# Kernel optimization log

Measured on AMD Instinct MI355X. Metric: run time of the kernel, lower is better.

The kernel has to match this reference:

```python
import jax, jax.numpy as jnp
import numpy as np

B, T, C, H = 2, 2048, 1024, 16
HD = C // H
EPS = 1e-5


def _gelu_tanh(x):
    # 0.5*x*(1+tanh(sqrt(2/pi)*(x+0.044715*x^3)))
    c = jnp.sqrt(jnp.asarray(2.0 / np.pi, dtype=x.dtype))
    return 0.5 * x * (1.0 + jnp.tanh(c * (x + 0.044715 * x * x * x)))


def _layernorm(x, g, b):
    mu = jnp.mean(x, axis=-1, keepdims=True)
    var = jnp.mean(jnp.square(x - mu), axis=-1, keepdims=True)
    return (x - mu) * jax.lax.rsqrt(var + EPS) * g + b


def setup_inputs() -> dict:
    key = jax.random.key(0)
    ks = jax.random.split(key, 8)
    s = lambda fan_in: 1.0 / np.sqrt(fan_in)
    return {
        "x": jax.random.normal(ks[0], (B, T, C), jnp.float32),
        "ln1_g": jnp.ones((C,), jnp.float32),
        "ln1_b": jnp.zeros((C,), jnp.float32),
        "W_attn": jax.random.normal(ks[1], (C, 3 * C), jnp.float32) * s(C),
        "b_attn": jnp.zeros((3 * C,), jnp.float32),
        "W_proj": jax.random.normal(ks[2], (C, C), jnp.float32) * s(C),
        "b_proj": jnp.zeros((C,), jnp.float32),
        "ln2_g": jnp.ones((C,), jnp.float32),
        "ln2_b": jnp.zeros((C,), jnp.float32),
        "W_fc": jax.random.normal(ks[3], (C, 4 * C), jnp.float32) * s(C),
        "b_fc": jnp.zeros((4 * C,), jnp.float32),
        "W_fc2": jax.random.normal(ks[4], (4 * C, C), jnp.float32) * s(4 * C),
        "b_fc2": jnp.zeros((C,), jnp.float32),
    }


def reference(x, ln1_g, ln1_b, W_attn, b_attn, W_proj, b_proj,
              ln2_g, ln2_b, W_fc, b_fc, W_fc2, b_fc2):
    # --- attention branch (pre-LN) ---
    h = _layernorm(x, ln1_g, ln1_b)
    qkv = h @ W_attn + b_attn                      # [B,T,3C]
    q, k, v = jnp.split(qkv, 3, axis=2)
    q = q.reshape(B, T, H, HD).transpose(0, 2, 1, 3)  # [B,H,T,HD]
    k = k.reshape(B, T, H, HD).transpose(0, 2, 1, 3)
    v = v.reshape(B, T, H, HD).transpose(0, 2, 1, 3)
    att = jnp.einsum('bhqd,bhkd->bhqk', q, k) / jnp.sqrt(jnp.asarray(HD, x.dtype))
    causal = jnp.tril(jnp.ones((T, T), bool))
    att = jnp.where(causal, att, jnp.asarray(-jnp.inf, att.dtype))
    att = jax.nn.softmax(att, axis=-1)
    y = jnp.einsum('bhqk,bhkd->bhqd', att, v)      # [B,H,T,HD]
    y = y.transpose(0, 2, 1, 3).reshape(B, T, C)
    x = x + (y @ W_proj + b_proj)
    # --- MLP branch (pre-LN) ---
    h = _layernorm(x, ln2_g, ln2_b)
    h = _gelu_tanh(h @ W_fc + b_fc)
    x = x + (h @ W_fc2 + b_fc2)
    return x
```

## Files before the change

kernel.cpp:

```cpp
#include <hip/hip_runtime.h>
#include <hip/hip_bf16.h>
#include <cstdint>
#include <cstddef>

#define B_  2
#define T_  2048
#define C_  1024
#define H_  16
#define HD_ 64
#define M_TOT 4096

typedef __bf16 bf16x8 __attribute__((ext_vector_type(8)));
typedef float  f32x4  __attribute__((ext_vector_type(4)));
typedef unsigned short u16;

__device__ __forceinline__ u16 f2bf(float f) {
  __hip_bfloat16 h = __float2bfloat16(f);
  return __builtin_bit_cast(u16, h);
}

__device__ __forceinline__ void async_cp16(const u16* g, u16* l) {
  __builtin_amdgcn_global_load_lds(
      (const __attribute__((address_space(1))) void*)g,
      (__attribute__((address_space(3))) void*)l, 16, 0, 0);
}

__device__ __forceinline__ float gelu_f(float x) {
  const float z = 0.7978845608028654f * (x + 0.044715f * x * x * x);
  return x / (1.0f + __expf(-2.0f * z));
}

__global__ __launch_bounds__(256) void ln_bf16_kernel(
    const float* __restrict__ x, const float* __restrict__ g,
    const float* __restrict__ b, u16* __restrict__ out) {
  const int row = blockIdx.x;
  const int tid = threadIdx.x;
  const float4 v = reinterpret_cast<const float4*>(x)[row * 256 + tid];
  float s  = v.x + v.y + v.z + v.w;
  float sq = v.x * v.x + v.y * v.y + v.z * v.z + v.w * v.w;
#pragma unroll
  for (int off = 32; off > 0; off >>= 1) {
    s  += __shfl_xor(s, off);
    sq += __shfl_xor(sq, off);
  }
  __shared__ float red[8];
  const int wave = tid >> 6;
  if ((tid & 63) == 0) { red[wave] = s; red[4 + wave] = sq; }
  __syncthreads();
  s  = red[0] + red[1] + red[2] + red[3];
  sq = red[4] + red[5] + red[6] + red[7];
  const float mu   = s * (1.0f / 1024.0f);
  const float rstd = rsqrtf(sq * (1.0f / 1024.0f) - mu * mu + 1e-5f);
  const float4 gv = reinterpret_cast<const float4*>(g)[tid];
  const float4 bv = reinterpret_cast<const float4*>(b)[tid];
  ushort4 o;
  o.x = f2bf((v.x - mu) * rstd * gv.x + bv.x);
  o.y = f2bf((v.y - mu) * rstd * gv.y + bv.y);
  o.z = f2bf((v.z - mu) * rstd * gv.z + bv.z);
  o.w = f2bf((v.w - mu) * rstd * gv.w + bv.w);
  reinterpret_cast<ushort4*>(out)[row * 256 + tid] = o;
}

__global__ __launch_bounds__(256) void transpose_bf16_kernel(
    const float* __restrict__ W, u16* __restrict__ Wt, int K, int N) {
  __shared__ float tile[32][33];
  const int n0 = blockIdx.x * 32, k0 = blockIdx.y * 32;
  const int tx = threadIdx.x & 31;
  const int ty = threadIdx.x >> 5;
#pragma unroll
  for (int i = 0; i < 4; ++i)
    tile[ty + 8 * i][tx] = W[(k0 + ty + 8 * i) * (size_t)N + n0 + tx];
  __syncthreads();
#pragma unroll
  for (int i = 0; i < 4; ++i)
    Wt[(n0 + ty + 8 * i) * (size_t)K + k0 + tx] = f2bf(tile[tx][ty + 8 * i]);
}

template <int MODE, int BM>
__global__ __launch_bounds__(256, 2) void gemm_kernel(
    const u16* __restrict__ A, const u16* __restrict__ Bt,
    const float* __restrict__ bias, const float* __restrict__ resid,
    float* __restrict__ outf, u16* __restrict__ outb,
    u16* __restrict__ qo, u16* __restrict__ ko, u16* __restrict__ vto,
    int M, int N, int K, int logPer) {
  constexpr int MT = BM / 32;
  constexpr int AI = BM / 32;
  __shared__ __align__(16) u16 As[BM * 64];
  __shared__ __align__(16) u16 Bs[128 * 64];
  const int tid  = threadIdx.x;
  const int wave = tid >> 6, lane = tid & 63;
  const int col  = lane & 15, quad = lane >> 4;
  const int wm   = wave >> 1, wn = wave & 1;

  const int flat = blockIdx.y * gridDim.x + blockIdx.x;
  const int xcd = flat & 7, sl = flat >> 3;
  const int per = 1 << logPer;
  const int bm = (xcd << logPer) + (sl & (per - 1));
  const int bn = sl >> logPer;

  const int srow = lane >> 3, sc8 = lane & 7;
  const int kcs = (sc8 ^ srow) * 8;
  const u16* ap = A  + (size_t)(bm * BM + wave * (BM / 4) + srow) * K + kcs;
  const u16* bp = Bt + (size_t)(bn * 128 + wave * 32 + srow) * K + kcs;
  u16* as_dst = As + wave * (BM / 4) * 64;
  u16* bs_dst = Bs + wave * 2048;

  f32x4 acc[MT][4] = {};

  for (int k0 = 0; k0 < K; k0 += 64) {
    __syncthreads();
#pragma unroll
    for (int i = 0; i < AI; ++i)
      async_cp16(ap + k0 + i * 8 * (size_t)K, as_dst + i * 512);
#pragma unroll
    for (int i = 0; i < 4; ++i)
      async_cp16(bp + k0 + i * 8 * (size_t)K, bs_dst + i * 512);
    __syncthreads();
#pragma unroll
    for (int kh = 0; kh < 2; ++kh) {
      const int ks = kh * 4;
      bf16x8 af[MT], bf[4];
#pragma unroll
      for (int mt = 0; mt < MT; ++mt) {
        const int row = wm * (BM / 2) + mt * 16 + col;
        af[mt] = *reinterpret_cast<const bf16x8*>(&As[row * 64 + ((ks + quad) ^ (col & 7)) * 8]);
      }
#pragma unroll
      for (int nt = 0; nt < 4; ++nt) {
        const int row = wn * 64 + nt * 16 + col;
        bf[nt] = *reinterpret_cast<const bf16x8*>(&Bs[row * 64 + ((ks + quad) ^ (col & 7)) * 8]);
      }
#pragma unroll
      for (int mt = 0; mt < MT; ++mt)
#pragma unroll
        for (int nt = 0; nt < 4; ++nt)
          acc[mt][nt] = __builtin_amdgcn_mfma_f32_16x16x32_bf16(af[mt], bf[nt], acc[mt][nt], 0, 0, 0);
    }
  }

#pragma unroll
  for (int mt = 0; mt < MT; ++mt) {
#pragma unroll
    for (int r = 0; r < 4; ++r) {
      const int grow = bm * BM + wm * (BM / 2) + mt * 16 + quad * 4 + r;
#pragma unroll
      for (int nt = 0; nt < 4; ++nt) {
        const int gcol = bn * 128 + wn * 64 + nt * 16 + col;
        const float val = acc[mt][nt][r] + bias[gcol];
        if constexpr (MODE == 0) {
          outb[(size_t)grow * N + gcol] = f2bf(gelu_f(val));
        } else if constexpr (MODE == 1) {
          outf[(size_t)grow * N + gcol] = resid[(size_t)grow * N + gcol] + val;
        } else {
          const int which = gcol >> 10, c = gcol & 1023;
          const int hh = c >> 6, dd = c & 63;
          const int bb = grow >> 11, tt = grow & 2047;
          if (which == 0)
            qo[((bb * H_ + hh) * (size_t)T_ + tt) * HD_ + dd] = f2bf(val * 0.125f);
          else if (which == 1)
            ko[((bb * H_ + hh) * (size_t)T_ + tt) * HD_ + dd] = f2bf(val);
          else
            vto[((bb * H_ + hh) * (size_t)HD_ + dd) * T_ + tt] = f2bf(val);
        }
      }
    }
  }
}

#define PSTR 68
__global__ __launch_bounds__(256, 4) void attn_kernel(
    const u16* __restrict__ q, const u16* __restrict__ k,
    const u16* __restrict__ vt, u16* __restrict__ y) {
  const int bh  = blockIdx.x;
  const int qt  = (T_ / 64 - 1) - blockIdx.y;
  const int tid = threadIdx.x;
  const int wave = tid >> 6, lane = tid & 63;
  const int col = lane & 15, quad = lane >> 4;
  const int b = bh >> 4, h = bh & 15;
  const int r0w = qt * 64 + wave * 16;

  __shared__ __align__(16) u16 Klds[64 * PSTR];
  __shared__ __align__(16) u16 Vtlds[64 * PSTR];
  __shared__ __align__(16) u16 Plds[4 * 16 * PSTR];

  bf16x8 aq[2];
#pragma unroll
  for (int j = 0; j < 2; ++j)
    aq[j] = *reinterpret_cast<const bf16x8*>(
        &q[((size_t)bh * T_ + r0w + col) * HD_ + j * 32 + quad * 8]);

  bf16x8 ones;
#pragma unroll
  for (int jj = 0; jj < 8; ++jj) ones[jj] = (__bf16)1.0f;

  f32x4 o[4] = {};
  f32x4 l_acc = {};

  const int srow = tid >> 3, spart = tid & 7;
  u16* pw = Plds + wave * 16 * PSTR;
  const u16* kbase  = k  + (size_t)bh * T_ * HD_ + srow * HD_ + spart * 8;
  const u16* vtbase = vt + (size_t)bh * HD_ * T_ + srow * T_ + spart * 8;

  const int kb_last = qt * 64;

  uint4 kv0, kv1, kv2, kv3;
  kv0 = *reinterpret_cast<const uint4*>(kbase);
  kv1 = *reinterpret_cast<const uint4*>(kbase + 32 * HD_);
  kv2 = *reinterpret_cast<const uint4*>(vtbase);
  kv3 = *reinterpret_cast<const uint4*>(vtbase + 32 * T_);

  for (int kb = 0; kb <= kb_last; kb += 64) {
    *reinterpret_cast<uint4*>(&Klds[srow * PSTR + spart * 8])        = kv0;
    *reinterpret_cast<uint4*>(&Klds[(srow + 32) * PSTR + spart * 8]) = kv1;
    *reinterpret_cast<uint4*>(&Vtlds[srow * PSTR + spart * 8])        = kv2;
    *reinterpret_cast<uint4*>(&Vtlds[(srow + 32) * PSTR + spart * 8]) = kv3;
    __syncthreads();

    if (kb < kb_last) {
      const int nk = kb + 64;
      kv0 = *reinterpret_cast<const uint4*>(kbase + (size_t)nk * HD_);
      kv1 = *reinterpret_cast<const uint4*>(kbase + (size_t)nk * HD_ + 32 * HD_);
      kv2 = *reinterpret_cast<const uint4*>(vtbase + nk);
      kv3 = *reinterpret_cast<const uint4*>(vtbase + 32 * T_ + nk);
    }

    f32x4 s[4];
#pragma unroll
    for (int n = 0; n < 4; ++n) {
      const bf16x8 bk0 = *reinterpret_cast<const bf16x8*>(&Klds[(n * 16 + col) * PSTR + quad * 8]);
      const bf16x8 bk1 = *reinterpret_cast<const bf16x8*>(&Klds[(n * 16 + col) * PSTR + 32 + quad * 8]);
      f32x4 z = {};
      z = __builtin_amdgcn_mfma_f32_16x16x32_bf16(aq[0], bk0, z, 0, 0, 0);
      s[n] = __builtin_amdgcn_mfma_f32_16x16x32_bf16(aq[1], bk1, z, 0, 0, 0);
    }

    const bool domask = (kb == kb_last);
#pragma unroll
    for (int n = 0; n < 4; ++n) {
#pragma unroll
      for (int r = 0; r < 4; ++r) {
        float sv = s[n][r];
        if (domask) {
          const int key = kb + n * 16 + col;
          const int row = r0w + quad * 4 + r;
          sv = (key <= row) ? sv : -1e30f;
        }
        pw[(quad * 4 + r) * PSTR + n * 16 + col] = f2bf(__expf(sv));
      }
    }
    __builtin_amdgcn_s_waitcnt(0xC07F);

    const bf16x8 ap0 = *reinterpret_cast<const bf16x8*>(&pw[col * PSTR + quad * 8]);
    const bf16x8 ap1 = *reinterpret_cast<const bf16x8*>(&pw[col * PSTR + 32 + quad * 8]);
    l_acc = __builtin_amdgcn_mfma_f32_16x16x32_bf16(ap0, ones, l_acc, 0, 0, 0);
    l_acc = __builtin_amdgcn_mfma_f32_16x16x32_bf16(ap1, ones, l_acc, 0, 0, 0);
#pragma unroll
    for (int n = 0; n < 4; ++n) {
      const bf16x8 bv0 = *reinterpret_cast<const bf16x8*>(&Vtlds[(n * 16 + col) * PSTR + quad * 8]);
      const bf16x8 bv1 = *reinterpret_cast<const bf16x8*>(&Vtlds[(n * 16 + col) * PSTR + 32 + quad * 8]);
      o[n] = __builtin_amdgcn_mfma_f32_16x16x32_bf16(ap0, bv0, o[n], 0, 0, 0);
      o[n] = __builtin_amdgcn_mfma_f32_16x16x32_bf16(ap1, bv1, o[n], 0, 0, 0);
    }
    __syncthreads();
  }

#pragma unroll
  for (int r = 0; r < 4; ++r) {
    const int qrow = r0w + quad * 4 + r;
    const float inv = 1.0f / l_acc[r];
#pragma unroll
    for (int n = 0; n < 4; ++n)
      y[((size_t)b * T_ + qrow) * C_ + h * HD_ + n * 16 + col] = f2bf(o[n][r] * inv);
  }
}

extern "C" void kernel_launch(void* const* d_in, const int* in_sizes, int n_in,
                              void* d_out, int out_size, void* d_ws, size_t ws_size,
                              hipStream_t stream) {
  const float* x      = (const float*)d_in[0];
  const float* ln1_g  = (const float*)d_in[1];
  const float* ln1_b  = (const float*)d_in[2];
  const float* W_attn = (const float*)d_in[3];
  const float* b_attn = (const float*)d_in[4];
  const float* W_proj = (const float*)d_in[5];
  const float* b_proj = (const float*)d_in[6];
  const float* ln2_g  = (const float*)d_in[7];
  const float* ln2_b  = (const float*)d_in[8];
  const float* W_fc   = (const float*)d_in[9];
  const float* b_fc   = (const float*)d_in[10];
  const float* W_fc2  = (const float*)d_in[11];
  const float* b_fc2  = (const float*)d_in[12];
  float* out = (float*)d_out;

  char* p = (char*)d_ws;
  auto alloc = [&](size_t bytes) {
    char* r = p;
    p += (bytes + 255) & ~(size_t)255;
    return r;
  };
  u16*   h1      = (u16*)alloc((size_t)M_TOT * C_ * 2);
  u16*   wt_attn = (u16*)alloc((size_t)3 * C_ * C_ * 2);
  u16*   wt_proj = (u16*)alloc((size_t)C_ * C_ * 2);
  u16*   wt_fc   = (u16*)alloc((size_t)4 * C_ * C_ * 2);
  u16*   wt_fc2  = (u16*)alloc((size_t)C_ * 4 * C_ * 2);
  u16*   qbuf    = (u16*)alloc((size_t)M_TOT * C_ * 2);
  u16*   kbuf    = (u16*)alloc((size_t)M_TOT * C_ * 2);
  u16*   vtbuf   = (u16*)alloc((size_t)M_TOT * C_ * 2);
  u16*   ybuf    = (u16*)alloc((size_t)M_TOT * C_ * 2);
  float* x2      = (float*)alloc((size_t)M_TOT * C_ * 4);
  u16*   h2      = (u16*)alloc((size_t)M_TOT * C_ * 2);
  u16*   act     = (u16*)alloc((size_t)M_TOT * 4 * C_ * 2);

  transpose_bf16_kernel<<<dim3(96, 32),  256, 0, stream>>>(W_attn, wt_attn, 1024, 3072);
  transpose_bf16_kernel<<<dim3(32, 32),  256, 0, stream>>>(W_proj, wt_proj, 1024, 1024);
  transpose_bf16_kernel<<<dim3(128, 32), 256, 0, stream>>>(W_fc,   wt_fc,   1024, 4096);
  transpose_bf16_kernel<<<dim3(32, 128), 256, 0, stream>>>(W_fc2,  wt_fc2,  4096, 1024);

  ln_bf16_kernel<<<M_TOT, 256, 0, stream>>>(x, ln1_g, ln1_b, h1);

  gemm_kernel<3, 128><<<dim3(24, 32), 256, 0, stream>>>(h1, wt_attn, b_attn, nullptr,
                                                        nullptr, nullptr, qbuf, kbuf, vtbuf,
                                                        4096, 3072, 1024, 2);
  attn_kernel<<<dim3(32, 32), 256, 0, stream>>>(qbuf, kbuf, vtbuf, ybuf);

  gemm_kernel<1, 64><<<dim3(8, 64), 256, 0, stream>>>(ybuf, wt_proj, b_proj, x,
                                                      x2, nullptr, nullptr, nullptr, nullptr,
                                                      4096, 1024, 1024, 3);
  ln_bf16_kernel<<<M_TOT, 256, 0, stream>>>(x2, ln2_g, ln2_b, h2);

  gemm_kernel<0, 128><<<dim3(32, 32), 256, 0, stream>>>(h2, wt_fc, b_fc, nullptr,
                                                        nullptr, act, nullptr, nullptr, nullptr,
                                                        4096, 4096, 1024, 2);
  gemm_kernel<1, 64><<<dim3(8, 64), 256, 0, stream>>>(act, wt_fc2, b_fc2, x2,
                                                      out, nullptr, nullptr, nullptr, nullptr,
                                                      4096, 1024, 4096, 3);
}
```

Before: 338.4 us.

## Load K and V tiles directly from global memory, drop shared staging

The attention kernel no longer stages K and V^T tiles through shared memory with block-wide barriers and register prefetch. Each wave now loads its MFMA operands for K and V^T straight from global memory, relying on L1/L2 to serve the four waves that read the same tile. This removes both __syncthreads per iteration and the LDS write/read traffic, and lowers occupancy hints from 4 to 3 blocks per SU. The cost is fourfold redundant global/cache traffic per block and no software prefetch, so load latency is exposed unless other waves hide it.

```diff
diff --git a/kernel.cpp b/kernel.cpp
--- a/kernel.cpp
+++ b/kernel.cpp
@@ -168,7 +168,7 @@
 }
 
 #define PSTR 68
-__global__ __launch_bounds__(256, 4) void attn_kernel(
+__global__ __launch_bounds__(256, 3) void attn_kernel(
     const u16* __restrict__ q, const u16* __restrict__ k,
     const u16* __restrict__ vt, u16* __restrict__ y) {
   const int bh  = blockIdx.x;
@@ -179,9 +179,8 @@
   const int b = bh >> 4, h = bh & 15;
   const int r0w = qt * 64 + wave * 16;
 
-  __shared__ __align__(16) u16 Klds[64 * PSTR];
-  __shared__ __align__(16) u16 Vtlds[64 * PSTR];
   __shared__ __align__(16) u16 Plds[4 * 16 * PSTR];
+  u16* pw = Plds + wave * 16 * PSTR;
 
   bf16x8 aq[2];
 #pragma unroll
@@ -196,42 +195,33 @@
   f32x4 o[4] = {};
   f32x4 l_acc = {};
 
-  const int srow = tid >> 3, spart = tid & 7;
-  u16* pw = Plds + wave * 16 * PSTR;
-  const u16* kbase  = k  + (size_t)bh * T_ * HD_ + srow * HD_ + spart * 8;
-  const u16* vtbase = vt + (size_t)bh * HD_ * T_ + srow * T_ + spart * 8;
+  const u16* kb_ptr = k  + ((size_t)bh * T_ + col) * HD_ + quad * 8;
+  const u16* vb_ptr = vt + ((size_t)bh * HD_ + col) * T_ + quad * 8;
 
   const int kb_last = qt * 64;
 
-  uint4 kv0, kv1, kv2, kv3;
-  kv0 = *reinterpret_cast<const uint4*>(kbase);
-  kv1 = *reinterpret_cast<const uint4*>(kbase + 32 * HD_);
-  kv2 = *reinterpret_cast<const uint4*>(vtbase);
-  kv3 = *reinterpret_cast<const uint4*>(vtbase + 32 * T_);
-
   for (int kb = 0; kb <= kb_last; kb += 64) {
-    *reinterpret_cast<uint4*>(&Klds[srow * PSTR + spart * 8])        = kv0;
-    *reinterpret_cast<uint4*>(&Klds[(srow + 32) * PSTR + spart * 8]) = kv1;
-    *reinterpret_cast<uint4*>(&Vtlds[srow * PSTR + spart * 8])        = kv2;
-    *reinterpret_cast<uint4*>(&Vtlds[(srow + 32) * PSTR + spart * 8]) = kv3;
-    __syncthreads();
-
-    if (kb < kb_last) {
-      const int nk = kb + 64;
-      kv0 = *reinterpret_cast<const uint4*>(kbase + (size_t)nk * HD_);
-      kv1 = *reinterpret_cast<const uint4*>(kbase + (size_t)nk * HD_ + 32 * HD_);
-      kv2 = *reinterpret_cast<const uint4*>(vtbase + nk);
-      kv3 = *reinterpret_cast<const uint4*>(vtbase + 32 * T_ + nk);
-    }
-
+    bf16x8 bk[4][2];
+#pragma unroll
+    for (int n = 0; n < 4; ++n) {
+      const u16* p = kb_ptr + (size_t)(kb + n * 16) * HD_;
+      bk[n][0] = *reinterpret_cast<const bf16x8*>(p);
+      bk[n][1] = *reinterpret_cast<const bf16x8*>(p + 32);
+    }
     f32x4 s[4];
 #pragma unroll
     for (int n = 0; n < 4; ++n) {
-      const bf16x8 bk0 = *reinterpret_cast<const bf16x8*>(&Klds[(n * 16 + col) * PSTR + quad * 8]);
-      const bf16x8 bk1 = *reinterpret_cast<const bf16x8*>(&Klds[(n * 16 + col) * PSTR + 32 + quad * 8]);
       f32x4 z = {};
-      z = __builtin_amdgcn_mfma_f32_16x16x32_bf16(aq[0], bk0, z, 0, 0, 0);
-      s[n] = __builtin_amdgcn_mfma_f32_16x16x32_bf16(aq[1], bk1, z, 0, 0, 0);
+      z = __builtin_amdgcn_mfma_f32_16x16x32_bf16(aq[0], bk[n][0], z, 0, 0, 0);
+      s[n] = __builtin_amdgcn_mfma_f32_16x16x32_bf16(aq[1], bk[n][1], z, 0, 0, 0);
+    }
+
+    bf16x8 bv[4][2];
+#pragma unroll
+    for (int n = 0; n < 4; ++n) {
+      const u16* p = vb_ptr + (size_t)(n * 16) * T_ + kb;
+      bv[n][0] = *reinterpret_cast<const bf16x8*>(p);
+      bv[n][1] = *reinterpret_cast<const bf16x8*>(p + 32);
     }
 
     const bool domask = (kb == kb_last);
@@ -256,12 +246,9 @@
     l_acc = __builtin_amdgcn_mfma_f32_16x16x32_bf16(ap1, ones, l_acc, 0, 0, 0);
 #pragma unroll
     for (int n = 0; n < 4; ++n) {
-      const bf16x8 bv0 = *reinterpret_cast<const bf16x8*>(&Vtlds[(n * 16 + col) * PSTR + quad * 8]);
-      const bf16x8 bv1 = *reinterpret_cast<const bf16x8*>(&Vtlds[(n * 16 + col) * PSTR + 32 + quad * 8]);
-      o[n] = __builtin_amdgcn_mfma_f32_16x16x32_bf16(ap0, bv0, o[n], 0, 0, 0);
-      o[n] = __builtin_amdgcn_mfma_f32_16x16x32_bf16(ap1, bv1, o[n], 0, 0, 0);
-    }
-    __syncthreads();
+      o[n] = __builtin_amdgcn_mfma_f32_16x16x32_bf16(ap0, bv[n][0], o[n], 0, 0, 0);
+      o[n] = __builtin_amdgcn_mfma_f32_16x16x32_bf16(ap1, bv[n][1], o[n], 0, 0, 0);
+    }
   }
 
 #pragma unroll
```

Result: slower. 428.9 us (+26.7%).

## Fuse weight transposes with LN1 into one prep kernel; transpose attention score MFMA

Applied to the files above, without the earlier changes.

The four weight-transpose launches and the first layernorm launch are merged into a single prep kernel that dispatches on block index, removing launch gaps and letting the pieces overlap. In attention, the QK^T MFMA operands are swapped so each lane holds four consecutive keys for one query row. The P tile can then be written to LDS as packed 8-byte stores instead of scalar 2-byte stores. The mask condition is widened to a per-wave test, which costs some extra compares on tiles that do not need masking.

```diff
diff --git a/kernel.cpp b/kernel.cpp
--- a/kernel.cpp
+++ b/kernel.cpp
@@ -30,11 +30,9 @@
   return x / (1.0f + __expf(-2.0f * z));
 }
 
-__global__ __launch_bounds__(256) void ln_bf16_kernel(
+__device__ __forceinline__ void ln_row(
     const float* __restrict__ x, const float* __restrict__ g,
-    const float* __restrict__ b, u16* __restrict__ out) {
-  const int row = blockIdx.x;
-  const int tid = threadIdx.x;
+    const float* __restrict__ b, u16* __restrict__ out, int row, int tid) {
   const float4 v = reinterpret_cast<const float4*>(x)[row * 256 + tid];
   float s  = v.x + v.y + v.z + v.w;
   float sq = v.x * v.x + v.y * v.y + v.z * v.z + v.w * v.w;
@@ -61,10 +59,29 @@
   reinterpret_cast<ushort4*>(out)[row * 256 + tid] = o;
 }
 
-__global__ __launch_bounds__(256) void transpose_bf16_kernel(
-    const float* __restrict__ W, u16* __restrict__ Wt, int K, int N) {
+__global__ __launch_bounds__(256) void ln_bf16_kernel(
+    const float* __restrict__ x, const float* __restrict__ g,
+    const float* __restrict__ b, u16* __restrict__ out) {
+  ln_row(x, g, b, out, blockIdx.x, threadIdx.x);
+}
+
+__global__ __launch_bounds__(256) void prep_kernel(
+    const float* __restrict__ x, const float* __restrict__ ln1_g,
+    const float* __restrict__ ln1_b, u16* __restrict__ h1,
+    const float* __restrict__ W_attn, u16* __restrict__ wt_attn,
+    const float* __restrict__ W_proj, u16* __restrict__ wt_proj,
+    const float* __restrict__ W_fc,   u16* __restrict__ wt_fc,
+    const float* __restrict__ W_fc2,  u16* __restrict__ wt_fc2) {
+  int bid = blockIdx.x;
+  if (bid < 4096) { ln_row(x, ln1_g, ln1_b, h1, bid, threadIdx.x); return; }
+  bid -= 4096;
+  const float* W; u16* Wt; int K, N, nx;
+  if (bid < 3072)      {              W = W_attn; Wt = wt_attn; K = 1024; N = 3072; nx = 96; }
+  else if (bid < 4096) { bid -= 3072; W = W_proj; Wt = wt_proj; K = 1024; N = 1024; nx = 32; }
+  else if (bid < 8192) { bid -= 4096; W = W_fc;   Wt = wt_fc;   K = 1024; N = 4096; nx = 128; }
+  else                 { bid -= 8192; W = W_fc2;  Wt = wt_fc2;  K = 4096; N = 1024; nx = 32; }
+  const int n0 = (bid % nx) * 32, k0 = (bid / nx) * 32;
   __shared__ float tile[32][33];
-  const int n0 = blockIdx.x * 32, k0 = blockIdx.y * 32;
   const int tx = threadIdx.x & 31;
   const int ty = threadIdx.x >> 5;
 #pragma unroll
@@ -182,12 +199,12 @@
   __shared__ __align__(16) u16 Klds[64 * PSTR];
   __shared__ __align__(16) u16 Vtlds[64 * PSTR];
   __shared__ __align__(16) u16 Plds[4 * 16 * PSTR];
-
-  bf16x8 aq[2];
-#pragma unroll
-  for (int j = 0; j < 2; ++j)
-    aq[j] = *reinterpret_cast<const bf16x8*>(
-        &q[((size_t)bh * T_ + r0w + col) * HD_ + j * 32 + quad * 8]);
+  u16* pw = Plds + wave * 16 * PSTR;
+
+  bf16x8 aq0 = *reinterpret_cast<const bf16x8*>(
+      &q[((size_t)bh * T_ + r0w + col) * HD_ + quad * 8]);
+  bf16x8 aq1 = *reinterpret_cast<const bf16x8*>(
+      &q[((size_t)bh * T_ + r0w + col) * HD_ + 32 + quad * 8]);
 
   bf16x8 ones;
 #pragma unroll
@@ -197,21 +214,19 @@
   f32x4 l_acc = {};
 
   const int srow = tid >> 3, spart = tid & 7;
-  u16* pw = Plds + wave * 16 * PSTR;
-  const u16* kbase  = k  + (size_t)bh * T_ * HD_ + srow * HD_ + spart * 8;
-  const u16* vtbase = vt + (size_t)bh * HD_ * T_ + srow * T_ + spart * 8;
+  const u16* kbase  = k  + (size_t)bh * T_ * HD_ + (size_t)srow * HD_ + spart * 8;
+  const u16* vtbase = vt + (size_t)bh * HD_ * T_ + (size_t)srow * T_ + spart * 8;
 
   const int kb_last = qt * 64;
 
-  uint4 kv0, kv1, kv2, kv3;
-  kv0 = *reinterpret_cast<const uint4*>(kbase);
-  kv1 = *reinterpret_cast<const uint4*>(kbase + 32 * HD_);
-  kv2 = *reinterpret_cast<const uint4*>(vtbase);
-  kv3 = *reinterpret_cast<const uint4*>(vtbase + 32 * T_);
+  uint4 kv0 = *reinterpret_cast<const uint4*>(kbase);
+  uint4 kv1 = *reinterpret_cast<const uint4*>(kbase + 32 * HD_);
+  uint4 kv2 = *reinterpret_cast<const uint4*>(vtbase);
+  uint4 kv3 = *reinterpret_cast<const uint4*>(vtbase + 32 * T_);
 
   for (int kb = 0; kb <= kb_last; kb += 64) {
-    *reinterpret_cast<uint4*>(&Klds[srow * PSTR + spart * 8])        = kv0;
-    *reinterpret_cast<uint4*>(&Klds[(srow + 32) * PSTR + spart * 8]) = kv1;
+    *reinterpret_cast<uint4*>(&Klds[srow * PSTR + spart * 8])         = kv0;
+    *reinterpret_cast<uint4*>(&Klds[(srow + 32) * PSTR + spart * 8])  = kv1;
     *reinterpret_cast<uint4*>(&Vtlds[srow * PSTR + spart * 8])        = kv2;
     *reinterpret_cast<uint4*>(&Vtlds[(srow + 32) * PSTR + spart * 8]) = kv3;
     __syncthreads();
@@ -224,29 +239,31 @@
       kv3 = *reinterpret_cast<const uint4*>(vtbase + 32 * T_ + nk);
     }
 
-    f32x4 s[4];
+    f32x4 st[4];
 #pragma unroll
     for (int n = 0; n < 4; ++n) {
-      const bf16x8 bk0 = *reinterpret_cast<const bf16x8*>(&Klds[(n * 16 + col) * PSTR + quad * 8]);
-      const bf16x8 bk1 = *reinterpret_cast<const bf16x8*>(&Klds[(n * 16 + col) * PSTR + 32 + quad * 8]);
+      const bf16x8 ak0 = *reinterpret_cast<const bf16x8*>(&Klds[(n * 16 + col) * PSTR + quad * 8]);
+      const bf16x8 ak1 = *reinterpret_cast<const bf16x8*>(&Klds[(n * 16 + col) * PSTR + 32 + quad * 8]);
       f32x4 z = {};
-      z = __builtin_amdgcn_mfma_f32_16x16x32_bf16(aq[0], bk0, z, 0, 0, 0);
-      s[n] = __builtin_amdgcn_mfma_f32_16x16x32_bf16(aq[1], bk1, z, 0, 0, 0);
-    }
-
-    const bool domask = (kb == kb_last);
+      z = __builtin_amdgcn_mfma_f32_16x16x32_bf16(ak0, aq0, z, 0, 0, 0);
+      st[n] = __builtin_amdgcn_mfma_f32_16x16x32_bf16(ak1, aq1, z, 0, 0, 0);
+    }
+
+    const bool domask = (kb + 63 > r0w);
 #pragma unroll
     for (int n = 0; n < 4; ++n) {
+      ushort4 pk;
 #pragma unroll
       for (int r = 0; r < 4; ++r) {
-        float sv = s[n][r];
+        float sv = st[n][r];
         if (domask) {
-          const int key = kb + n * 16 + col;
-          const int row = r0w + quad * 4 + r;
+          const int key = kb + n * 16 + quad * 4 + r;
+          const int row = r0w + col;
           sv = (key <= row) ? sv : -1e30f;
         }
-        pw[(quad * 4 + r) * PSTR + n * 16 + col] = f2bf(__expf(sv));
+        reinterpret_cast<u16*>(&pk)[r] = f2bf(__expf(sv));
       }
+      *reinterpret_cast<ushort4*>(&pw[col * PSTR + n * 16 + quad * 4]) = pk;
     }
     __builtin_amdgcn_s_waitcnt(0xC07F);
 
@@ -311,12 +328,9 @@
   u16*   h2      = (u16*)alloc((size_t)M_TOT * C_ * 2);
   u16*   act     = (u16*)alloc((size_t)M_TOT * 4 * C_ * 2);
 
-  transpose_bf16_kernel<<<dim3(96, 32),  256, 0, stream>>>(W_attn, wt_attn, 1024, 3072);
-  transpose_bf16_kernel<<<dim3(32, 32),  256, 0, stream>>>(W_proj, wt_proj, 1024, 1024);
-  transpose_bf16_kernel<<<dim3(128, 32), 256, 0, stream>>>(W_fc,   wt_fc,   1024, 4096);
-  transpose_bf16_kernel<<<dim3(32, 128), 256, 0, stream>>>(W_fc2,  wt_fc2,  4096, 1024);
-
-  ln_bf16_kernel<<<M_TOT, 256, 0, stream>>>(x, ln1_g, ln1_b, h1);
+  prep_kernel<<<16384, 256, 0, stream>>>(x, ln1_g, ln1_b, h1,
+                                         W_attn, wt_attn, W_proj, wt_proj,
+                                         W_fc, wt_fc, W_fc2, wt_fc2);
 
   gemm_kernel<3, 128><<<dim3(24, 32), 256, 0, stream>>>(h1, wt_attn, b_attn, nullptr,
                                                         nullptr, nullptr, qbuf, kbuf, vtbuf,
```

Measured after the change: 327.2 us. 3.3% less time.
